# Kernel tuning notes

Hardware: AMD Instinct MI355X
Metric: run time of the kernel (lower is better)

## Reference

```python
import jax, jax.numpy as jnp
import numpy as np

B, T, U, V = 16, 160, 80, 512  # U+1 = 81 joint label rows; blank = V-1 (torchaudio blank=-1)


def setup_inputs() -> dict:
    key = jax.random.key(0)
    k1, k2, k3, k4 = jax.random.split(key, 4)
    logits = jax.random.normal(k1, (B, T, U + 1, V), dtype=jnp.float32)
    targets = jax.random.randint(k2, (B, U), 0, V - 1, dtype=jnp.int32)  # labels never equal blank
    logit_lengths = jax.random.randint(k3, (B,), T // 2, T + 1, dtype=jnp.int32)
    target_lengths = jax.random.randint(k4, (B,), U // 2, U + 1, dtype=jnp.int32)
    # ensure at least one sample uses the full lattice
    logit_lengths = logit_lengths.at[0].set(T)
    target_lengths = target_lengths.at[0].set(U)
    return {
        "logits": logits,
        "targets": targets,
        "logit_lengths": logit_lengths,
        "target_lengths": target_lengths,
    }


def _rnnt_loss(logits, targets, logit_lengths, target_lengths):
    b_, t_, u1, v = logits.shape
    u_ = u1 - 1
    lp = jax.nn.log_softmax(logits, axis=-1)            # [B,T,U+1,V]
    blank_lp = lp[..., v - 1]                            # [B,T,U+1], blank = last index
    lab_lp = jnp.take_along_axis(
        lp[:, :, :u_, :], targets[:, None, :, None].astype(jnp.int32), axis=3
    )[..., 0]                                            # [B,T,U]

    # alpha[t,u] = logaddexp(alpha[t-1,u] + blank[t-1,u], alpha[t,u-1] + label[t,u-1])
    # t = 0 row: emit first u labels at frame 0
    row0 = jnp.concatenate(
        [jnp.zeros((b_, 1), lp.dtype), jnp.cumsum(lab_lp[:, 0, :], axis=-1)], axis=1
    )  # [B, U+1]

    def t_step(prev_row, xs):
        blank_prev, lab_t = xs                # [B,U+1], [B,U]
        base = prev_row + blank_prev          # came-from-below term
        x0 = base[:, 0]                       # u = 0: only blank path

        def u_step(x, inp):
            b_u, a_u = inp                    # each [B]
            x_new = jnp.logaddexp(b_u, x + a_u)
            return x_new, x_new

        _, ys = jax.lax.scan(u_step, x0, (base[:, 1:].T, lab_t.T))  # [U,B]
        row = jnp.concatenate([x0[:, None], ys.T], axis=1)          # [B,U+1]
        return row, row

    blank_seq = jnp.moveaxis(blank_lp[:, :-1, :], 1, 0)  # [T-1,B,U+1] (blank at t-1)
    lab_seq = jnp.moveaxis(lab_lp[:, 1:, :], 1, 0)       # [T-1,B,U]
    _, rows = jax.lax.scan(t_step, row0, (blank_seq, lab_seq))
    alpha = jnp.concatenate([row0[None], rows], axis=0)  # [T,B,U+1]
    alpha = jnp.moveaxis(alpha, 0, 1)                    # [B,T,U+1]

    bi = jnp.arange(b_)
    t_idx = logit_lengths.astype(jnp.int32) - 1
    u_idx = target_lengths.astype(jnp.int32)
    log_like = alpha[bi, t_idx, u_idx] + blank_lp[bi, t_idx, u_idx]
    return jnp.mean(-log_like)  # torchaudio default reduction='mean'


def reference(logits, targets, logit_lengths, target_lengths):
    return _rnnt_loss(logits, targets, logit_lengths, target_lengths)
```

## Files before the change

### kernel.cpp

```cpp
#include <hip/hip_runtime.h>

#define L2E 1.4426950408889634f
#define LN2 0.6931471805599453f
#define NEG (-1e30f)

constexpr int Bc = 16, Tc = 160, Uc = 80, U1 = 81, Vc = 512, DD = 240;

__device__ __forceinline__ float laddexp(float a, float b) {
    float m = fmaxf(a, b);
    float d = fminf(a, b) - m;
    float e = __builtin_amdgcn_exp2f(d * L2E);
    return fmaf(LN2, __builtin_amdgcn_logf(1.0f + e), m);
}

__global__ __launch_bounds__(256) void k_lse(const float* __restrict__ logits,
                                             const int* __restrict__ targets,
                                             float* __restrict__ blankD,
                                             float* __restrict__ labD) {
    const int lane = threadIdx.x & 63;
    const int wid  = threadIdx.x >> 6;
    const int r    = blockIdx.x * 4 + wid;
    const int u    = r % U1;
    const int bt   = r / U1;
    const int t    = bt % Tc;
    const int b    = bt / Tc;

    const float* __restrict__ row = logits + (size_t)r * Vc;
    const float4 x0 = reinterpret_cast<const float4*>(row)[lane];
    const float4 x1 = reinterpret_cast<const float4*>(row)[lane + 64];

    float m = fmaxf(fmaxf(fmaxf(x0.x, x0.y), fmaxf(x0.z, x0.w)),
                    fmaxf(fmaxf(x1.x, x1.y), fmaxf(x1.z, x1.w)));
#pragma unroll
    for (int o = 32; o; o >>= 1) m = fmaxf(m, __shfl_xor(m, o));

    float s = __builtin_amdgcn_exp2f((x0.x - m) * L2E)
            + __builtin_amdgcn_exp2f((x0.y - m) * L2E)
            + __builtin_amdgcn_exp2f((x0.z - m) * L2E)
            + __builtin_amdgcn_exp2f((x0.w - m) * L2E)
            + __builtin_amdgcn_exp2f((x1.x - m) * L2E)
            + __builtin_amdgcn_exp2f((x1.y - m) * L2E)
            + __builtin_amdgcn_exp2f((x1.z - m) * L2E)
            + __builtin_amdgcn_exp2f((x1.w - m) * L2E);
#pragma unroll
    for (int o = 32; o; o >>= 1) s += __shfl_xor(s, o);

    if (lane == 0) {
        const float lse = fmaf(LN2, __builtin_amdgcn_logf(s), m);
        const int sidx = t + u;
        const size_t idx = ((size_t)b * DD + sidx) * U1 + u;
        blankD[idx] = row[Vc - 1] - lse;
        if (u < Uc) {
            labD[idx] = row[targets[b * Uc + u]] - lse;
        }
    }
}

__global__ __launch_bounds__(64) void k_dp(const float* __restrict__ blankD,
                                           const float* __restrict__ labD,
                                           const int* __restrict__ llen,
                                           const int* __restrict__ tlen,
                                           float* __restrict__ loss) {
    const int b    = blockIdx.x;
    const int lane = threadIdx.x;
    const int u0 = 2 * lane, u1 = u0 + 1;
    const bool v0 = (u0 <= Uc), v1 = (u1 <= Uc);
    const int cu0  = v0 ? u0 : Uc;
    const int cu1  = v1 ? u1 : Uc;
    const int cu0m = (cu0 >= 1) ? (cu0 - 1) : 0;

    const float* __restrict__ bl = blankD + (size_t)b * DD * U1;
    const float* __restrict__ la = labD  + (size_t)b * DD * U1;
    const int tl = llen[b], ul = tlen[b];
    const int d_end = tl - 1 + ul;

    float a0 = (u0 == 0) ? 0.0f : NEG;
    float a1 = NEG;
    float res = NEG;

    float pb0[8], pb1[8], pl0[8], pl1[8];
#pragma unroll
    for (int k = 0; k < 8; ++k) {
        pb0[k] = bl[k * U1 + cu0];
        pb1[k] = bl[k * U1 + cu1];
        pl0[k] = la[k * U1 + cu0m];
        pl1[k] = la[k * U1 + cu0];
    }

    for (int g = 0; g < 30; ++g) {
        const int dbase = 1 + g * 8;
        float nb0[8], nb1[8], nl0[8], nl1[8];
#pragma unroll
        for (int k = 0; k < 8; ++k) {
            int s = dbase + 7 + k;
            if (s > DD - 1) s = DD - 1;
            nb0[k] = bl[s * U1 + cu0];
            nb1[k] = bl[s * U1 + cu1];
            nl0[k] = la[s * U1 + cu0m];
            nl1[k] = la[s * U1 + cu0];
        }
#pragma unroll
        for (int k = 0; k < 8; ++k) {
            const int d = dbase + k;
            const float a1m = __shfl_up(a1, 1);
            const int t0 = d - u0, t1 = d - u1;
            float top0 = (t0 >= 1) ? (a0 + pb0[k]) : NEG;
            float lef0 = (u0 >= 1) ? (a1m + pl0[k]) : NEG;
            float top1 = (t1 >= 1) ? (a1 + pb1[k]) : NEG;
            float lef1 = a0 + pl1[k];
            float na0 = laddexp(top0, lef0);
            float na1 = laddexp(top1, lef1);
            na0 = (v0 && t0 >= 0 && t0 < Tc) ? na0 : NEG;
            na1 = (v1 && t1 >= 0 && t1 < Tc) ? na1 : NEG;
            a0 = na0; a1 = na1;
            if (d == d_end) {
                if (u0 == ul) res = a0 + bl[d * U1 + u0];
                if (u1 == ul) res = a1 + bl[d * U1 + u1];
            }
        }
#pragma unroll
        for (int k = 0; k < 8; ++k) {
            pb0[k] = nb0[k]; pb1[k] = nb1[k]; pl0[k] = nl0[k]; pl1[k] = nl1[k];
        }
    }
    if (u0 == ul || u1 == ul) loss[b] = -res;
}

__global__ __launch_bounds__(64) void k_final(const float* __restrict__ loss,
                                              float* __restrict__ out) {
    float s = (threadIdx.x < Bc) ? loss[threadIdx.x] : 0.0f;
#pragma unroll
    for (int o = 32; o; o >>= 1) s += __shfl_xor(s, o);
    if (threadIdx.x == 0) out[0] = s * (1.0f / Bc);
}

extern "C" void kernel_launch(void* const* d_in, const int* in_sizes, int n_in,
                              void* d_out, int out_size, void* d_ws, size_t ws_size,
                              hipStream_t stream) {
    const float* logits  = (const float*)d_in[0];
    const int*   targets = (const int*)d_in[1];
    const int*   llen    = (const int*)d_in[2];
    const int*   tlen    = (const int*)d_in[3];

    float* ws     = (float*)d_ws;
    float* blankD = ws;
    float* labD   = ws + (size_t)Bc * DD * U1;
    float* loss   = labD + (size_t)Bc * DD * U1;
    float* out    = (float*)d_out;

    const int nrows = Bc * Tc * U1;
    k_lse<<<dim3(nrows / 4), dim3(256), 0, stream>>>(logits, targets, blankD, labD);
    k_dp<<<dim3(Bc), dim3(64), 0, stream>>>(blankD, labD, llen, tlen, loss);
    k_final<<<dim3(1), dim3(64), 0, stream>>>(loss, out);
}
```

Before: 561.9 us.

## Process two rows per wave in LSE and fold final mean into DP kernel

```diff
diff --git a/kernel.cpp b/kernel.cpp
--- a/kernel.cpp
+++ b/kernel.cpp
@@ -16,42 +16,68 @@
 __global__ __launch_bounds__(256) void k_lse(const float* __restrict__ logits,
                                              const int* __restrict__ targets,
                                              float* __restrict__ blankD,
-                                             float* __restrict__ labD) {
+                                             float* __restrict__ labD,
+                                             int* __restrict__ counter) {
+    if (blockIdx.x == 0 && threadIdx.x == 0) *counter = 0;
     const int lane = threadIdx.x & 63;
     const int wid  = threadIdx.x >> 6;
-    const int r    = blockIdx.x * 4 + wid;
-    const int u    = r % U1;
-    const int bt   = r / U1;
-    const int t    = bt % Tc;
-    const int b    = bt / Tc;
+    const int r0   = blockIdx.x * 8 + wid * 2;
 
-    const float* __restrict__ row = logits + (size_t)r * Vc;
-    const float4 x0 = reinterpret_cast<const float4*>(row)[lane];
-    const float4 x1 = reinterpret_cast<const float4*>(row)[lane + 64];
+    const float4* __restrict__ bp =
+        reinterpret_cast<const float4*>(logits + (size_t)r0 * Vc);
+    const float4 a0 = bp[lane];
+    const float4 a1 = bp[lane + 64];
+    const float4 b0 = bp[lane + 128];
+    const float4 b1 = bp[lane + 192];
 
-    float m = fmaxf(fmaxf(fmaxf(x0.x, x0.y), fmaxf(x0.z, x0.w)),
-                    fmaxf(fmaxf(x1.x, x1.y), fmaxf(x1.z, x1.w)));
+    float m0 = fmaxf(fmaxf(fmaxf(a0.x, a0.y), fmaxf(a0.z, a0.w)),
+                     fmaxf(fmaxf(a1.x, a1.y), fmaxf(a1.z, a1.w)));
+    float m1 = fmaxf(fmaxf(fmaxf(b0.x, b0.y), fmaxf(b0.z, b0.w)),
+                     fmaxf(fmaxf(b1.x, b1.y), fmaxf(b1.z, b1.w)));
 #pragma unroll
-    for (int o = 32; o; o >>= 1) m = fmaxf(m, __shfl_xor(m, o));
+    for (int o = 32; o; o >>= 1) {
+        m0 = fmaxf(m0, __shfl_xor(m0, o));
+        m1 = fmaxf(m1, __shfl_xor(m1, o));
+    }
+    const float k0 = m0 * L2E, k1 = m1 * L2E;
+    float s0 = __builtin_amdgcn_exp2f(fmaf(a0.x, L2E, -k0))
+             + __builtin_amdgcn_exp2f(fmaf(a0.y, L2E, -k0))
+             + __builtin_amdgcn_exp2f(fmaf(a0.z, L2E, -k0))
+             + __builtin_amdgcn_exp2f(fmaf(a0.w, L2E, -k0))
+             + __builtin_amdgcn_exp2f(fmaf(a1.x, L2E, -k0))
+             + __builtin_amdgcn_exp2f(fmaf(a1.y, L2E, -k0))
+             + __builtin_amdgcn_exp2f(fmaf(a1.z, L2E, -k0))
+             + __builtin_amdgcn_exp2f(fmaf(a1.w, L2E, -k0));
+    float s1 = __builtin_amdgcn_exp2f(fmaf(b0.x, L2E, -k1))
+             + __builtin_amdgcn_exp2f(fmaf(b0.y, L2E, -k1))
+             + __builtin_amdgcn_exp2f(fmaf(b0.z, L2E, -k1))
+             + __builtin_amdgcn_exp2f(fmaf(b0.w, L2E, -k1))
+             + __builtin_amdgcn_exp2f(fmaf(b1.x, L2E, -k1))
+             + __builtin_amdgcn_exp2f(fmaf(b1.y, L2E, -k1))
+             + __builtin_amdgcn_exp2f(fmaf(b1.z, L2E, -k1))
+             + __builtin_amdgcn_exp2f(fmaf(b1.w, L2E, -k1));
+#pragma unroll
+    for (int o = 32; o; o >>= 1) {
+        s0 += __shfl_xor(s0, o);
+        s1 += __shfl_xor(s1, o);
+    }
 
-    float s = __builtin_amdgcn_exp2f((x0.x - m) * L2E)
-            + __builtin_amdgcn_exp2f((x0.y - m) * L2E)
-            + __builtin_amdgcn_exp2f((x0.z - m) * L2E)
-            + __builtin_amdgcn_exp2f((x0.w - m) * L2E)
-            + __builtin_amdgcn_exp2f((x1.x - m) * L2E)
-            + __builtin_amdgcn_exp2f((x1.y - m) * L2E)
-            + __builtin_amdgcn_exp2f((x1.z - m) * L2E)
-            + __builtin_amdgcn_exp2f((x1.w - m) * L2E);
-#pragma unroll
-    for (int o = 32; o; o >>= 1) s += __shfl_xor(s, o);
-
-    if (lane == 0) {
+    const float bl0 = __shfl(a1.w, 63);
+    const float bl1 = __shfl(b1.w, 63);
+    if (lane < 2) {
+        const int r = r0 + lane;
+        const float m = lane ? m1 : m0;
+        const float s = lane ? s1 : s0;
+        const float blank_logit = lane ? bl1 : bl0;
         const float lse = fmaf(LN2, __builtin_amdgcn_logf(s), m);
-        const int sidx = t + u;
-        const size_t idx = ((size_t)b * DD + sidx) * U1 + u;
-        blankD[idx] = row[Vc - 1] - lse;
+        const int u  = r % U1;
+        const int bt = r / U1;
+        const int t  = bt % Tc;
+        const int b  = bt / Tc;
+        const size_t idx = ((size_t)b * DD + (t + u)) * U1 + u;
+        blankD[idx] = blank_logit - lse;
         if (u < Uc) {
-            labD[idx] = row[targets[b * Uc + u]] - lse;
+            labD[idx] = logits[(size_t)r * Vc + targets[b * Uc + u]] - lse;
         }
     }
 }
@@ -60,7 +86,9 @@
                                            const float* __restrict__ labD,
                                            const int* __restrict__ llen,
                                            const int* __restrict__ tlen,
-                                           float* __restrict__ loss) {
+                                           float* __restrict__ loss,
+                                           int* __restrict__ counter,
+                                           float* __restrict__ out) {
     const int b    = blockIdx.x;
     const int lane = threadIdx.x;
     const int u0 = 2 * lane, u1 = u0 + 1;
@@ -73,6 +101,9 @@
     const float* __restrict__ la = labD  + (size_t)b * DD * U1;
     const int tl = llen[b], ul = tlen[b];
     const int d_end = tl - 1 + ul;
+    const float end_blank = bl[(size_t)d_end * U1 + ul];
+    const int lane_e = ul >> 1;
+    const int slot1  = ul & 1;
 
     float a0 = (u0 == 0) ? 0.0f : NEG;
     float a1 = NEG;
@@ -114,8 +145,8 @@
             na1 = (v1 && t1 >= 0 && t1 < Tc) ? na1 : NEG;
             a0 = na0; a1 = na1;
             if (d == d_end) {
-                if (u0 == ul) res = a0 + bl[d * U1 + u0];
-                if (u1 == ul) res = a1 + bl[d * U1 + u1];
+                const float av = slot1 ? a1 : a0;
+                if (lane == lane_e) res = av + end_blank;
             }
         }
 #pragma unroll
@@ -123,15 +154,19 @@
             pb0[k] = nb0[k]; pb1[k] = nb1[k]; pl0[k] = nl0[k]; pl1[k] = nl1[k];
         }
     }
-    if (u0 == ul || u1 == ul) loss[b] = -res;
-}
 
-__global__ __launch_bounds__(64) void k_final(const float* __restrict__ loss,
-                                              float* __restrict__ out) {
-    float s = (threadIdx.x < Bc) ? loss[threadIdx.x] : 0.0f;
+    if (lane == lane_e) loss[b] = -res;
+    __threadfence();
+    if (lane == 0) {
+        const int old = __hip_atomic_fetch_add(counter, 1, __ATOMIC_ACQ_REL,
+                                               __HIP_MEMORY_SCOPE_AGENT);
+        if (old == Bc - 1) {
+            float s = 0.0f;
 #pragma unroll
-    for (int o = 32; o; o >>= 1) s += __shfl_xor(s, o);
-    if (threadIdx.x == 0) out[0] = s * (1.0f / Bc);
+            for (int i = 0; i < Bc; ++i) s += loss[i];
+            out[0] = s * (1.0f / Bc);
+        }
+    }
 }
 
 extern "C" void kernel_launch(void* const* d_in, const int* in_sizes, int n_in,
@@ -146,10 +181,10 @@
     float* blankD = ws;
     float* labD   = ws + (size_t)Bc * DD * U1;
     float* loss   = labD + (size_t)Bc * DD * U1;
+    int*   counter = (int*)(loss + Bc);
     float* out    = (float*)d_out;
 
     const int nrows = Bc * Tc * U1;
-    k_lse<<<dim3(nrows / 4), dim3(256), 0, stream>>>(logits, targets, blankD, labD);
-    k_dp<<<dim3(Bc), dim3(64), 0, stream>>>(blankD, labD, llen, tlen, loss);
-    k_final<<<dim3(1), dim3(64), 0, stream>>>(loss, out);
+    k_lse<<<dim3(nrows / 8), dim3(256), 0, stream>>>(logits, targets, blankD, labD, counter);
+    k_dp<<<dim3(Bc), dim3(64), 0, stream>>>(blankD, labD, llen, tlen, loss, counter, out);
 }
```

After: 570.7 us. No clear change (+1.6%).
